# Kernel tuning notes

Measured on AMD Instinct MI355X. Metric: run time of the kernel, lower is better.

The kernel has to match this reference:

```python
import jax, jax.numpy as jnp
import numpy as np

N, T, C, H, W = 4, 8, 512, 14, 14
HEADS = 8
D = C // HEADS            # 64 per-head dim
S = T * H * W             # 1568 sequence length
EPS = 1e-8
NEG = -2.0**32 + 1.0      # padding value used by the original module


def setup_inputs() -> dict:
    key = jax.random.key(0)
    ks = jax.random.split(key, 8)
    shp = (N, T, C, H, W)
    scale = 1.0 / np.sqrt(C)
    return {
        "queries": jax.random.normal(ks[0], shp, jnp.float32),
        "keys": jax.random.normal(ks[1], shp, jnp.float32),
        "values": jax.random.normal(ks[2], shp, jnp.float32),
        "Wq": jax.random.normal(ks[3], (C, C), jnp.float32) * scale,
        "bq": jnp.zeros((C,), jnp.float32),
        "Wk": jax.random.normal(ks[4], (C, C), jnp.float32) * scale,
        "bk": jnp.zeros((C,), jnp.float32),
        "Wv": jax.random.normal(ks[5], (C, C), jnp.float32) * scale,
        "bv": jnp.zeros((C,), jnp.float32),
        "gamma": jnp.ones((C,), jnp.float32),
        "beta": jnp.zeros((C,), jnp.float32),
    }


def _proj(x, Wt, b):
    # 1x1 Conv2d + ReLU over channel dim of (N, T, C, H, W)
    y = jnp.einsum('ntchw,oc->ntohw', x, Wt) + b[None, None, :, None, None]
    return jax.nn.relu(y)


def _flatten(x):
    # (N, T, C, H, W) -> (N, T*H*W, C)
    return x.transpose(0, 1, 3, 4, 2).reshape(N, S, C)


def _split_heads(x):
    # torch.cat(torch.chunk(x, HEADS, dim=2), dim=0): (N, S, C) -> (HEADS*N, S, D)
    return x.reshape(N, S, HEADS, D).transpose(2, 0, 1, 3).reshape(HEADS * N, S, D)


def reference(queries, keys, values, Wq, bq, Wk, bk, Wv, bv, gamma, beta):
    Qf = _flatten(_proj(queries, Wq, bq))
    Kf = _flatten(_proj(keys, Wk, bk))
    Vf = _flatten(_proj(values, Wv, bv))
    q_flat = _flatten(queries)   # residual + query mask source
    k_flat = _flatten(keys)      # key mask source

    Q_ = _split_heads(Qf)
    K_ = _split_heads(Kf)
    V_ = _split_heads(Vf)

    scores = jnp.einsum('bqd,bkd->bqk', Q_, K_) / jnp.sqrt(jnp.float32(D))

    # key padding mask: sign(|sum over C|), tiled over heads -> (HEADS*N, 1, S)
    key_mask = jnp.sign(jnp.abs(k_flat.sum(-1)))          # (N, S)
    km = jnp.tile(key_mask, (HEADS, 1))[:, None, :]
    scores = jnp.where(km == 0.0, NEG, scores)

    attn = jax.nn.softmax(scores, axis=-1)

    # query padding mask (multiplicative) -> (HEADS*N, S, 1)
    query_mask = jnp.sign(jnp.abs(q_flat.sum(-1)))        # (N, S)
    qm = jnp.tile(query_mask, (HEADS, 1))[:, :, None]
    attn = attn * qm

    out = jnp.einsum('bqk,bkd->bqd', attn, V_)
    # merge heads back: inverse of _split_heads
    out = out.reshape(HEADS, N, S, D).transpose(1, 2, 0, 3).reshape(N, S, C)

    out = out + q_flat  # residual

    # custom LayerNorm: torch .std() is unbiased (ddof=1)
    mean = out.mean(-1, keepdims=True)
    std = jnp.sqrt(out.var(-1, ddof=1, keepdims=True))
    out = gamma * (out - mean) / (std + EPS) + beta

    # reshape back to (N, T, C, H, W)
    return out.reshape(N, T, H, W, C).transpose(0, 1, 4, 2, 3)
```

## Files before the change

kernel.cpp:

```cpp
#include <hip/hip_runtime.h>
#include <math.h>

#define N_ 4
#define T_ 8
#define C_ 512
#define H_ 14
#define W_ 14
#define HEADS_ 8
#define D_ 64
#define HW_ 196
#define S_ 1568
#define P_TOT 6272
#define KMP_ 1600
#define NEGL_ (-1.0e38f)
#define EPS_ 1e-8f
#define QSC_ 0.18033688011112042f

typedef __attribute__((ext_vector_type(8))) short short8v;
typedef __attribute__((ext_vector_type(4))) float float4v;
typedef __attribute__((ext_vector_type(4))) unsigned short ushort4v;
typedef unsigned short ushort_t;

__device__ __forceinline__ ushort_t f2bf(float f) {
    union { float f; unsigned u; } a; a.f = f;
    unsigned r = (a.u + 0x7FFFu + ((a.u >> 16) & 1u)) >> 16;
    return (ushort_t)r;
}
__device__ __forceinline__ float bf2f(ushort_t u) {
    union { unsigned u; float f; } t; t.u = ((unsigned)u) << 16; return t.f;
}
__device__ __forceinline__ unsigned cvt_pk_bf16(float lo, float hi) {
    unsigned r;
    asm("v_cvt_pk_bf16_f32 %0, %1, %2" : "=v"(r) : "v"(lo), "v"(hi));
    return r;
}
__device__ __forceinline__ float exp2_fast(float x) {
    float r;
    asm("v_exp_f32 %0, %1" : "=v"(r) : "v"(x));
    return r;
}
__device__ __forceinline__ float max3f(float a, float b, float c) {
    float r;
    asm("v_max3_f32 %0, %1, %2, %3" : "=v"(r) : "v"(a), "v"(b), "v"(c));
    return r;
}
__device__ __forceinline__ float4v mfma16(short8v a, short8v b, float4v c) {
    return __builtin_amdgcn_mfma_f32_16x16x32_bf16(a, b, c, 0, 0, 0);
}
__device__ __forceinline__ void gload_lds16(const void* g, void* l) {
    __builtin_amdgcn_global_load_lds(
        (const __attribute__((address_space(1))) unsigned int*)g,
        (__attribute__((address_space(3))) unsigned int*)l,
        16, 0, 0);
}
__device__ __forceinline__ void gload_lds4(const void* g, void* l) {
    __builtin_amdgcn_global_load_lds(
        (const __attribute__((address_space(1))) unsigned int*)g,
        (__attribute__((address_space(3))) unsigned int*)l,
        4, 0, 0);
}

__global__ __launch_bounds__(256) void transpose_kernel(
    const float* __restrict__ q_in, const float* __restrict__ k_in,
    const float* __restrict__ v_in, ushort_t* __restrict__ qbf,
    ushort_t* __restrict__ kbf, ushort_t* __restrict__ vbf)
{
    __shared__ float Xs[64][197];
    const int z = blockIdx.z;
    const float* src = (z == 0) ? q_in : (z == 1) ? k_in : v_in;
    ushort_t* dst = (z == 0) ? qbf : (z == 1) ? kbf : vbf;

    const int nt = blockIdx.x;
    const int ct = blockIdx.y;
    const int tid = threadIdx.x;

    const long gbase = ((long)nt * C_ + ct * 64) * HW_;
    #pragma unroll
    for (int i = 0; i < 13; ++i) {
        const int idx = i * 256 + tid;
        if (idx < 3136) {
            const int c = idx / 49;
            const int q4 = idx - c * 49;
            const float4 v = *(const float4*)(src + gbase + c * HW_ + q4 * 4);
            Xs[c][q4 * 4 + 0] = v.x;
            Xs[c][q4 * 4 + 1] = v.y;
            Xs[c][q4 * 4 + 2] = v.z;
            Xs[c][q4 * 4 + 3] = v.w;
        }
    }
    __syncthreads();
    const long pbase = (long)nt * HW_;
    const int c0 = (tid & 15) * 4;
    #pragma unroll
    for (int i = 0; i < 13; ++i) {
        const int idx = i * 256 + tid;
        if (idx < 3136) {
            const int hw = idx >> 4;
            ushort4v pk;
            #pragma unroll
            for (int e = 0; e < 4; ++e) pk[e] = f2bf(Xs[c0 + e][hw]);
            *(ushort4v*)(dst + (pbase + hw) * C_ + ct * 64 + c0) = pk;
        }
    }
}

__global__ __launch_bounds__(256) void wconv_kernel(
    const float* __restrict__ Wq, const float* __restrict__ Wk,
    const float* __restrict__ Wv, ushort_t* __restrict__ Wbf)
{
    const int z = blockIdx.y;
    const float* src = (z == 0) ? Wq : (z == 1) ? Wk : Wv;
    const int q = blockIdx.x * 256 + threadIdx.x;
    const float4 v = *(const float4*)(src + q * 4);
    ushort4v pk;
    pk[0] = f2bf(v.x); pk[1] = f2bf(v.y); pk[2] = f2bf(v.z); pk[3] = f2bf(v.w);
    *(ushort4v*)(Wbf + (long)z * 262144 + q * 4) = pk;
}

__global__ __launch_bounds__(256) void mask_kernel(
    const ushort_t* __restrict__ qbf, const ushort_t* __restrict__ kbf,
    float* __restrict__ qm, float* __restrict__ km)
{
    const int tid = threadIdx.x;
    const int w = tid >> 6, lane = tid & 63;
    const int p = blockIdx.x * 4 + w;
    const short8v qv = *(const short8v*)(qbf + (long)p * C_ + lane * 8);
    const short8v kv = *(const short8v*)(kbf + (long)p * C_ + lane * 8);
    float sq = 0.f, sk = 0.f;
    #pragma unroll
    for (int j = 0; j < 8; ++j) {
        sq += bf2f(((const ushort_t*)&qv)[j]);
        sk += bf2f(((const ushort_t*)&kv)[j]);
    }
    #pragma unroll
    for (int off = 32; off > 0; off >>= 1) {
        sq += __shfl_xor(sq, off, 64);
        sk += __shfl_xor(sk, off, 64);
    }
    if (lane == 0) {
        const int n = p / S_, s = p - n * S_;
        qm[p] = (sq != 0.f) ? 1.f : 0.f;
        km[n * KMP_ + s] = (sk != 0.f) ? 0.f : NEGL_;
    }
    if (blockIdx.x == 0 && tid < 128) {
        const int nn = tid >> 5;
        const int ss = S_ + (tid & 31);
        km[nn * KMP_ + ss] = NEGL_;
    }
}

__global__ __launch_bounds__(256) void proj_all(
    const ushort_t* __restrict__ qbf, const ushort_t* __restrict__ kbf,
    const ushort_t* __restrict__ vbf, const ushort_t* __restrict__ Wbf,
    const float* __restrict__ bq, const float* __restrict__ bk,
    const float* __restrict__ bv,
    ushort_t* __restrict__ Qh, ushort_t* __restrict__ Kh,
    ushort_t* __restrict__ Vt)
{
    __shared__ char lds[24576];

    const int fid = blockIdx.x;
    const int xcd = fid & 7;
    const int iin = fid >> 3;
    const int v = xcd * 147 + iin;
    const int z = v / 392;
    const int rem = v - z * 392;
    const int ptile = rem >> 3;
    const int head = rem & 7;

    const ushort_t* Xbf = (z == 0) ? qbf : (z == 1) ? kbf : vbf;
    const ushort_t* Wz = Wbf + (long)z * 262144;
    const float* bias = (z == 0) ? bq : (z == 1) ? bk : bv;
    ushort_t* outp = (z == 0) ? Qh : (z == 1) ? Kh : Vt;
    const bool TR = (z == 2);
    const float osc = (z == 0) ? QSC_ : 1.0f;

    const int tid = threadIdx.x;
    const int w = tid >> 6, lane = tid & 63, lg = lane >> 4, lo = lane & 15;
    const int wr = w >> 1, wc = w & 1;
    const int p0 = ptile * 128;
    const int o0 = head * 64;

    char* Xl = lds;
    char* Wl = lds + 16384;
    const int wbase = (tid & 192) * 16;

    float4v acc[2][4];
    #pragma unroll
    for (int a = 0; a < 2; ++a)
        #pragma unroll
        for (int b = 0; b < 4; ++b) acc[a][b] = (float4v){0.f, 0.f, 0.f, 0.f};

    auto stage = [&](int k0) {
        #pragma unroll
        for (int i = 0; i < 4; ++i) {
            const int sl = tid + i * 256;
            const int row = sl >> 3, sir = sl & 7;
            const int c16 = sir ^ (row & 7);
            gload_lds16(Xbf + (long)(p0 + row) * C_ + k0 + c16 * 8,
                        Xl + i * 4096 + wbase);
        }
        #pragma unroll
        for (int i = 0; i < 2; ++i) {
            const int sl = tid + i * 256;
            const int row = sl >> 3, sir = sl & 7;
            const int c16 = sir ^ (row & 7);
            gload_lds16(Wz + (long)(o0 + row) * C_ + k0 + c16 * 8,
                        Wl + i * 4096 + wbase);
        }
    };

    for (int kstep = 0; kstep < 8; ++kstep) {
        stage(kstep * 64);
        __syncthreads();

        short8v wf[2][2], xf[4][2];
        #pragma unroll
        for (int a = 0; a < 2; ++a) {
            const int row = wc * 32 + a * 16 + lo;
            const int swr = (row & 7) << 4;
            #pragma unroll
            for (int ks = 0; ks < 2; ++ks) {
                const int base = row * 128 + ks * 64 + lg * 8;
                ((uint2*)&wf[a][ks])[0] = *(const uint2*)(Wl + (base ^ swr));
                ((uint2*)&wf[a][ks])[1] = *(const uint2*)(Wl + ((base + 32) ^ swr));
            }
        }
        #pragma unroll
        for (int b = 0; b < 4; ++b) {
            const int row = wr * 64 + b * 16 + lo;
            const int swr = (row & 7) << 4;
            #pragma unroll
            for (int ks = 0; ks < 2; ++ks) {
                const int base = row * 128 + ks * 64 + lg * 8;
                ((uint2*)&xf[b][ks])[0] = *(const uint2*)(Xl + (base ^ swr));
                ((uint2*)&xf[b][ks])[1] = *(const uint2*)(Xl + ((base + 32) ^ swr));
            }
        }
        __builtin_amdgcn_s_setprio(1);
        if (!TR) {
            #pragma unroll
            for (int ks = 0; ks < 2; ++ks)
                #pragma unroll
                for (int a = 0; a < 2; ++a)
                    #pragma unroll
                    for (int b = 0; b < 4; ++b)
                        acc[a][b] = mfma16(wf[a][ks], xf[b][ks], acc[a][b]);
        } else {
            #pragma unroll
            for (int ks = 0; ks < 2; ++ks)
                #pragma unroll
                for (int a = 0; a < 2; ++a)
                    #pragma unroll
                    for (int b = 0; b < 4; ++b)
                        acc[a][b] = mfma16(xf[b][ks], wf[a][ks], acc[a][b]);
        }
        __builtin_amdgcn_s_setprio(0);
        __syncthreads();
    }

    if (!TR) {
        #pragma unroll
        for (int b = 0; b < 4; ++b) {
            const int p = p0 + wr * 64 + b * 16 + lo;
            const int nb = p / S_;
            const int s = p - nb * S_;
            #pragma unroll
            for (int a = 0; a < 2; ++a) {
                const int d0 = wc * 32 + a * 16 + lg * 4;
                const float4v bs = *(const float4v*)(bias + o0 + d0);
                ushort4v pk;
                #pragma unroll
                for (int e = 0; e < 4; ++e) {
                    float vv = acc[a][b][e] + bs[e];
                    vv = vv > 0.f ? vv : 0.f;
                    pk[e] = f2bf(vv * osc);
                }
                *(ushort4v*)(outp + ((long)(head * N_ + nb) * S_ + s) * D_ + d0) = pk;
            }
        }
    } else {
        #pragma unroll
        for (int a = 0; a < 2; ++a) {
            const int d = wc * 32 + a * 16 + lo;
            const float bsc = bias[o0 + d];
            #pragma unroll
            for (int b = 0; b < 4; ++b) {
                const int pb = p0 + wr * 64 + b * 16 + lg * 4;
                const int nb = pb / S_;
                const int s0 = pb - nb * S_;
                ushort4v pk;
                #pragma unroll
                for (int e = 0; e < 4; ++e) {
                    float vv = acc[a][b][e] + bsc;
                    vv = vv > 0.f ? vv : 0.f;
                    pk[e] = f2bf(vv);
                }
                *(ushort4v*)(outp + ((long)(head * N_ + nb) * D_ + d) * S_ + s0) = pk;
            }
        }
    }
}

__global__ __launch_bounds__(256) void attn_kernel(
    const ushort_t* __restrict__ Qh, const ushort_t* __restrict__ Kh,
    const ushort_t* __restrict__ Vt, const float* __restrict__ km,
    ushort_t* __restrict__ Pc, float* __restrict__ Ml)
{
    __shared__ char lds[16384 + 256];

    const int tid = threadIdx.x;
    const int lane = tid & 63;
    const int w = tid >> 6;
    const int lg = lane >> 4;
    const int lo = lane & 15;

    const int split = blockIdx.y;
    const int t1 = 7 + split * 6;
    const int t0 = split ? (1 + split * 6) : 0;

    const int fid = blockIdx.x;
    const int x = fid & 7;
    const int j = fid >> 3;
    const int b = x + 8 * (j / 25);
    const int q0 = (j % 25) * 64;
    const int n = b & (N_ - 1);

    char* Kl = lds;
    char* Vl = lds + 8192;
    const float* kms = (const float*)(lds + 16384);
    const int wbase = (tid & 192) * 16;

    const int qrow = q0 + w * 16 + lo;
    const int qcl = qrow < S_ ? qrow : S_ - 1;
    const ushort_t* qp = Qh + ((long)b * S_ + qcl) * D_ + lg * 4;
    short8v qf[2];
    #pragma unroll
    for (int ks = 0; ks < 2; ++ks) {
        ((uint2*)&qf[ks])[0] = *(const uint2*)(qp + ks * 32);
        ((uint2*)&qf[ks])[1] = *(const uint2*)(qp + ks * 32 + 16);
    }

    float4v acc[4];
    #pragma unroll
    for (int dt = 0; dt < 4; ++dt) acc[dt] = (float4v){0.f, 0.f, 0.f, 0.f};
    float m_run = -INFINITY, l_run = 0.f;

    auto stage = [&](int kb) {
        #pragma unroll
        for (int i = 0; i < 2; ++i) {
            const int s = i * 256 + tid;
            const int row = s >> 3;
            const int c16 = (s & 7) ^ (row & 7);
            int krow = kb + row; if (krow >= S_) krow = S_ - 1;
            gload_lds16(Kh + ((long)b * S_ + krow) * D_ + c16 * 8,
                        Kl + i * 4096 + wbase);
        }
        #pragma unroll
        for (int i = 0; i < 2; ++i) {
            const int s = i * 256 + tid;
            const int row = s >> 3;
            const int c16 = (s & 7) ^ (row & 7);
            int kc = kb + c16 * 8; if (kc > S_ - 8) kc = S_ - 8;
            gload_lds16(Vt + ((long)b * D_ + row) * S_ + kc,
                        Vl + i * 4096 + wbase);
        }
        if (w == 0)
            gload_lds4(km + (long)n * KMP_ + kb + lane, (void*)kms);
    };

    for (int t = t0; t < t1; ++t) {
        stage(t * 64);
        __syncthreads();

        float4v s[4];
        __builtin_amdgcn_s_setprio(1);
        #pragma unroll
        for (int kt = 0; kt < 4; ++kt) {
            s[kt] = (float4v){0.f, 0.f, 0.f, 0.f};
            #pragma unroll
            for (int ks = 0; ks < 2; ++ks) {
                const int row = kt * 16 + lo;
                const int base = row * 128 + ks * 64 + lg * 8;
                const int swr = (row & 7) << 4;
                short8v kf;
                ((uint2*)&kf)[0] = *(const uint2*)(Kl + (base ^ swr));
                ((uint2*)&kf)[1] = *(const uint2*)(Kl + ((base + 32) ^ swr));
                s[kt] = mfma16(kf, qf[ks], s[kt]);
            }
        }
        __builtin_amdgcn_s_setprio(0);

        float p[4][4];
        #pragma unroll
        for (int kt = 0; kt < 4; ++kt) {
            const float4v bv4 = *(const float4v*)&kms[kt * 16 + lg * 4];
            #pragma unroll
            for (int r = 0; r < 4; ++r) p[kt][r] = s[kt][r] + bv4[r];
        }
        const float m1 = max3f(p[0][0], p[0][1], p[0][2]);
        const float m2 = max3f(p[0][3], p[1][0], p[1][1]);
        const float m3 = max3f(p[1][2], p[1][3], p[2][0]);
        const float m4 = max3f(p[2][1], p[2][2], p[2][3]);
        const float m5 = max3f(p[3][0], p[3][1], p[3][2]);
        float mx = max3f(max3f(m1, m2, m3), m4, fmaxf(m5, p[3][3]));
        mx = fmaxf(mx, __shfl_xor(mx, 16, 64));
        mx = fmaxf(mx, __shfl_xor(mx, 32, 64));
        float mn;
        if (__all(mx <= m_run + 8.f)) {
            mn = m_run;
        } else {
            mn = fmaxf(m_run, mx);
            const float alpha = exp2_fast(m_run - mn);
            m_run = mn;
            l_run *= alpha;
            #pragma unroll
            for (int dt = 0; dt < 4; ++dt)
                #pragma unroll
                for (int r = 0; r < 4; ++r) acc[dt][r] *= alpha;
        }
        float rs4[4];
        #pragma unroll
        for (int kt = 0; kt < 4; ++kt) {
            #pragma unroll
            for (int r = 0; r < 4; ++r) p[kt][r] = exp2_fast(p[kt][r] - mn);
            rs4[kt] = (p[kt][0] + p[kt][1]) + (p[kt][2] + p[kt][3]);
        }
        l_run += (rs4[0] + rs4[1]) + (rs4[2] + rs4[3]);

        short8v pf[2];
        #pragma unroll
        for (int kt = 0; kt < 4; ++kt) {
            const unsigned w0 = cvt_pk_bf16(p[kt][0], p[kt][1]);
            const unsigned w1 = cvt_pk_bf16(p[kt][2], p[kt][3]);
            ((unsigned*)&pf[kt >> 1])[(kt & 1) * 2] = w0;
            ((unsigned*)&pf[kt >> 1])[(kt & 1) * 2 + 1] = w1;
        }

        __builtin_amdgcn_s_setprio(1);
        #pragma unroll
        for (int dt = 0; dt < 4; ++dt) {
            #pragma unroll
            for (int ks = 0; ks < 2; ++ks) {
                const int row = dt * 16 + lo;
                const int base = row * 128 + ks * 64 + lg * 8;
                const int swr = (row & 7) << 4;
                short8v vf;
                ((uint2*)&vf)[0] = *(const uint2*)(Vl + (base ^ swr));
                ((uint2*)&vf)[1] = *(const uint2*)(Vl + ((base + 32) ^ swr));
                acc[dt] = mfma16(vf, pf[ks], acc[dt]);
            }
        }
        __builtin_amdgcn_s_setprio(0);
        __syncthreads();
    }

    l_run += __shfl_xor(l_run, 16, 64);
    l_run += __shfl_xor(l_run, 32, 64);

    if (qrow < S_) {
        const long rbase = ((long)split * 32 + b) * S_ + qrow;
        if (lg == 0) {
            Ml[rbase * 2] = m_run;
            Ml[rbase * 2 + 1] = l_run;
        }
        ushort_t* P = Pc + rbase * 64;
        #pragma unroll
        for (int dt = 0; dt < 4; ++dt) {
            uint2 uu;
            uu.x = cvt_pk_bf16(acc[dt][0], acc[dt][1]);
            uu.y = cvt_pk_bf16(acc[dt][2], acc[dt][3]);
            *(uint2*)(P + dt * 16 + lg * 4) = uu;
        }
    }
}

__global__ __launch_bounds__(256) void combine_stats_kernel(
    const ushort_t* __restrict__ Pc, const float* __restrict__ Ml,
    const float* __restrict__ qm, const ushort_t* __restrict__ qbf,
    ushort_t* __restrict__ Om, float* __restrict__ stats)
{
    const int tid = threadIdx.x;
    const int wv = tid >> 6, lane = tid & 63;
    const long pos = (long)blockIdx.x * 4 + wv;
    const int n = (int)(pos / S_);
    const int q = (int)(pos - (long)n * S_);
    const int head = lane >> 3;
    const int d0 = (lane & 7) * 8;

    long rb[4];
    float mv[4], lv[4];
    float M = -INFINITY;
    #pragma unroll
    for (int s = 0; s < 4; ++s) {
        rb[s] = ((long)(s * 32 + head * 4 + n) * S_ + q);
        const float2 ml = *(const float2*)(Ml + rb[s] * 2);
        mv[s] = ml.x; lv[s] = ml.y;
        M = fmaxf(M, ml.x);
    }
    float L = 0.f;
    float o[8] = {0.f, 0.f, 0.f, 0.f, 0.f, 0.f, 0.f, 0.f};
    #pragma unroll
    for (int s = 0; s < 4; ++s) {
        const float wgt = exp2_fast(mv[s] - M);
        L = fmaf(lv[s], wgt, L);
        const ushort4v a0 = *(const ushort4v*)(Pc + rb[s] * 64 + d0);
        const ushort4v a1 = *(const ushort4v*)(Pc + rb[s] * 64 + d0 + 4);
        #pragma unroll
        for (int e = 0; e < 4; ++e) {
            o[e] = fmaf(bf2f(a0[e]), wgt, o[e]);
            o[4 + e] = fmaf(bf2f(a1[e]), wgt, o[4 + e]);
        }
    }
    L = fmaxf(L, 1e-20f);
    const float scale = qm[pos] / L;
    const short8v qv = *(const short8v*)(qbf + pos * C_ + lane * 8);
    ushort4v ov0, ov1;
    float sum = 0.f, ssq = 0.f;
    #pragma unroll
    for (int e = 0; e < 8; ++e) {
        const ushort_t ob = f2bf(o[e] * scale);
        if (e < 4) ov0[e] = ob; else ov1[e - 4] = ob;
        const float v = bf2f(ob) + bf2f(((const ushort_t*)&qv)[e]);
        sum += v; ssq += v * v;
    }
    #pragma unroll
    for (int off = 32; off > 0; off >>= 1) {
        sum += __shfl_xor(sum, off, 64);
        ssq += __shfl_xor(ssq, off, 64);
    }
    *(ushort4v*)(Om + pos * C_ + lane * 8) = ov0;
    *(ushort4v*)(Om + pos * C_ + lane * 8 + 4) = ov1;
    if (lane == 0) {
        const float mean = sum * (1.f / 512.f);
        float var = (ssq - sum * mean) * (1.f / 511.f);
        var = var > 0.f ? var : 0.f;
        stats[pos * 2] = mean;
        stats[pos * 2 + 1] = 1.f / (sqrtf(var) + EPS_);
    }
}

__global__ __launch_bounds__(256) void ln_write_kernel(
    const ushort_t* __restrict__ Om, const ushort_t* __restrict__ qbf,
    const float* __restrict__ stats, const float* __restrict__ gamma,
    const float* __restrict__ beta, float* __restrict__ out)
{
    __shared__ float Tl[64][197];
    const int nt = blockIdx.x;
    const int ct = blockIdx.y;
    const int tid = threadIdx.x;

    const int c0 = (tid & 15) * 4;
    float g[4], bb[4];
    #pragma unroll
    for (int e = 0; e < 4; ++e) {
        g[e] = gamma[ct * 64 + c0 + e];
        bb[e] = beta[ct * 64 + c0 + e];
    }

    #pragma unroll
    for (int i = 0; i < 13; ++i) {
        const int idx = i * 256 + tid;
        if (idx < 3136) {
            const int hw = idx >> 4;
            const long p = (long)nt * HW_ + hw;
            const float mean = stats[p * 2];
            const float inv = stats[p * 2 + 1];
            const ushort4v ov = *(const ushort4v*)(Om + p * C_ + ct * 64 + c0);
            const ushort4v qv = *(const ushort4v*)(qbf + p * C_ + ct * 64 + c0);
            #pragma unroll
            for (int e = 0; e < 4; ++e) {
                const float xv = bf2f(ov[e]) + bf2f(qv[e]);
                Tl[c0 + e][hw] = g[e] * (xv - mean) * inv + bb[e];
            }
        }
    }
    __syncthreads();
    const long obase = ((long)nt * C_ + ct * 64) * HW_;
    #pragma unroll
    for (int i = 0; i < 13; ++i) {
        const int idx = i * 256 + tid;
        if (idx < 3136) {
            const int c = idx / 49;
            const int q4 = idx - c * 49;
            float4 v;
            v.x = Tl[c][q4 * 4 + 0];
            v.y = Tl[c][q4 * 4 + 1];
            v.z = Tl[c][q4 * 4 + 2];
            v.w = Tl[c][q4 * 4 + 3];
            *(float4*)(out + obase + c * HW_ + q4 * 4) = v;
        }
    }
}

extern "C" void kernel_launch(void* const* d_in, const int* in_sizes, int n_in,
                              void* d_out, int out_size, void* d_ws, size_t ws_size,
                              hipStream_t stream) {
    const float* q_in  = (const float*)d_in[0];
    const float* k_in  = (const float*)d_in[1];
    const float* v_in  = (const float*)d_in[2];
    const float* Wq    = (const float*)d_in[3];
    const float* bq    = (const float*)d_in[4];
    const float* Wk    = (const float*)d_in[5];
    const float* bk    = (const float*)d_in[6];
    const float* Wv    = (const float*)d_in[7];
    const float* bv    = (const float*)d_in[8];
    const float* gamma = (const float*)d_in[9];
    const float* beta  = (const float*)d_in[10];
    float* out = (float*)d_out;

    const size_t PC = (size_t)P_TOT * C_;
    ushort_t* qbf = (ushort_t*)d_ws;
    ushort_t* kbf = qbf + PC;
    ushort_t* vbf = kbf + PC;
    ushort_t* Wbf = vbf + PC;
    ushort_t* Qh  = Wbf + 3 * (size_t)C_ * C_;
    ushort_t* Kh  = Qh + PC;
    ushort_t* Vt  = Kh + PC;
    ushort_t* Om  = Vt + PC;
    ushort_t* Pc  = Om + PC;
    float* Ml    = (float*)(Pc + 4L * 32 * S_ * 64);
    float* stats = Ml + 4L * 32 * S_ * 2;
    float* qm    = stats + 2 * P_TOT;
    float* km    = qm + P_TOT;

    transpose_kernel<<<dim3(32, 8, 3), 256, 0, stream>>>(q_in, k_in, v_in, qbf, kbf, vbf);
    wconv_kernel<<<dim3(256, 3), 256, 0, stream>>>(Wq, Wk, Wv, Wbf);
    mask_kernel<<<P_TOT / 4, 256, 0, stream>>>(qbf, kbf, qm, km);
    proj_all<<<1176, 256, 0, stream>>>(qbf, kbf, vbf, Wbf, bq, bk, bv, Qh, Kh, Vt);
    attn_kernel<<<dim3(800, 4), 256, 0, stream>>>(Qh, Kh, Vt, km, Pc, Ml);
    combine_stats_kernel<<<P_TOT / 4, 256, 0, stream>>>(Pc, Ml, qm, qbf, Om, stats);
    ln_write_kernel<<<dim3(32, 8), 256, 0, stream>>>(Om, qbf, stats, gamma, beta, out);
}
```

Before: 103.7 us.

## Double-buffer K/V tiles in attention kernel and preload key mask once

Attention kernel now uses two LDS buffers for K and V, issuing the async global-to-LDS load for the next key tile before computing on the current one, with one barrier per tile. The key-mask bias for the block's whole key range is loaded into LDS once at kernel start rather than per tile. Swizzled LDS fragment offsets are precomputed once. The goal is to hide global load latency behind MFMA work; the cost is doubled LDS use, which may reduce occupancy.

```diff
diff --git a/kernel.cpp b/kernel.cpp
--- a/kernel.cpp
+++ b/kernel.cpp
@@ -53,12 +53,6 @@
         (__attribute__((address_space(3))) unsigned int*)l,
         16, 0, 0);
 }
-__device__ __forceinline__ void gload_lds4(const void* g, void* l) {
-    __builtin_amdgcn_global_load_lds(
-        (const __attribute__((address_space(1))) unsigned int*)g,
-        (__attribute__((address_space(3))) unsigned int*)l,
-        4, 0, 0);
-}
 
 __global__ __launch_bounds__(256) void transpose_kernel(
     const float* __restrict__ q_in, const float* __restrict__ k_in,
@@ -307,7 +301,7 @@
     const ushort_t* __restrict__ Vt, const float* __restrict__ km,
     ushort_t* __restrict__ Pc, float* __restrict__ Ml)
 {
-    __shared__ char lds[16384 + 256];
+    __shared__ char lds[2 * 16384 + 1792];
 
     const int tid = threadIdx.x;
     const int lane = tid & 63;
@@ -326,10 +320,17 @@
     const int q0 = (j % 25) * 64;
     const int n = b & (N_ - 1);
 
-    char* Kl = lds;
-    char* Vl = lds + 8192;
-    const float* kms = (const float*)(lds + 16384);
     const int wbase = (tid & 192) * 16;
+    float* kml = (float*)(lds + 32768);
+
+    {
+        const int nt = (t1 - t0) * 64;
+        #pragma unroll
+        for (int i = 0; i < 2; ++i) {
+            const int idx = i * 256 + tid;
+            if (idx < nt) kml[idx] = km[(long)n * KMP_ + t0 * 64 + idx];
+        }
+    }
 
     const int qrow = q0 + w * 16 + lo;
     const int qcl = qrow < S_ ? qrow : S_ - 1;
@@ -346,7 +347,12 @@
     for (int dt = 0; dt < 4; ++dt) acc[dt] = (float4v){0.f, 0.f, 0.f, 0.f};
     float m_run = -INFINITY, l_run = 0.f;
 
-    auto stage = [&](int kb) {
+    const int swr = (lo & 7) << 4;
+    const int fo[2][2] = {
+        { ((lg * 8) ^ swr) + lo * 128,      ((lg * 8 + 32) ^ swr) + lo * 128 },
+        { ((64 + lg * 8) ^ swr) + lo * 128, ((64 + lg * 8 + 32) ^ swr) + lo * 128 } };
+
+    auto stage = [&](char* Kb, char* Vb, int kb) {
         #pragma unroll
         for (int i = 0; i < 2; ++i) {
             const int s = i * 256 + tid;
@@ -354,7 +360,7 @@
             const int c16 = (s & 7) ^ (row & 7);
             int krow = kb + row; if (krow >= S_) krow = S_ - 1;
             gload_lds16(Kh + ((long)b * S_ + krow) * D_ + c16 * 8,
-                        Kl + i * 4096 + wbase);
+                        Kb + i * 4096 + wbase);
         }
         #pragma unroll
         for (int i = 0; i < 2; ++i) {
@@ -363,15 +369,15 @@
             const int c16 = (s & 7) ^ (row & 7);
             int kc = kb + c16 * 8; if (kc > S_ - 8) kc = S_ - 8;
             gload_lds16(Vt + ((long)b * D_ + row) * S_ + kc,
-                        Vl + i * 4096 + wbase);
-        }
-        if (w == 0)
-            gload_lds4(km + (long)n * KMP_ + kb + lane, (void*)kms);
+                        Vb + i * 4096 + wbase);
+        }
     };
 
-    for (int t = t0; t < t1; ++t) {
-        stage(t * 64);
-        __syncthreads();
+    char* K0 = lds;             char* V0 = lds + 8192;
+    char* K1 = lds + 16384;     char* V1 = lds + 24576;
+
+    auto compute = [&](const char* Kl, const char* Vl, int t) {
+        const float* kms = kml + (t - t0) * 64;
 
         float4v s[4];
         __builtin_amdgcn_s_setprio(1);
@@ -380,12 +386,9 @@
             s[kt] = (float4v){0.f, 0.f, 0.f, 0.f};
             #pragma unroll
             for (int ks = 0; ks < 2; ++ks) {
-                const int row = kt * 16 + lo;
-                const int base = row * 128 + ks * 64 + lg * 8;
-                const int swr = (row & 7) << 4;
                 short8v kf;
-                ((uint2*)&kf)[0] = *(const uint2*)(Kl + (base ^ swr));
-                ((uint2*)&kf)[1] = *(const uint2*)(Kl + ((base + 32) ^ swr));
+                ((uint2*)&kf)[0] = *(const uint2*)(Kl + kt * 2048 + fo[ks][0]);
+                ((uint2*)&kf)[1] = *(const uint2*)(Kl + kt * 2048 + fo[ks][1]);
                 s[kt] = mfma16(kf, qf[ks], s[kt]);
             }
         }
@@ -442,17 +445,24 @@
         for (int dt = 0; dt < 4; ++dt) {
             #pragma unroll
             for (int ks = 0; ks < 2; ++ks) {
-                const int row = dt * 16 + lo;
-                const int base = row * 128 + ks * 64 + lg * 8;
-                const int swr = (row & 7) << 4;
                 short8v vf;
-                ((uint2*)&vf)[0] = *(const uint2*)(Vl + (base ^ swr));
-                ((uint2*)&vf)[1] = *(const uint2*)(Vl + ((base + 32) ^ swr));
+                ((uint2*)&vf)[0] = *(const uint2*)(Vl + dt * 2048 + fo[ks][0]);
+                ((uint2*)&vf)[1] = *(const uint2*)(Vl + dt * 2048 + fo[ks][1]);
                 acc[dt] = mfma16(vf, pf[ks], acc[dt]);
             }
         }
         __builtin_amdgcn_s_setprio(0);
+    };
+
+    stage(K0, V0, t0 * 64);
+    for (int t = t0; t < t1; t += 2) {
         __syncthreads();
+        if (t + 1 < t1) stage(K1, V1, (t + 1) * 64);
+        compute(K0, V0, t);
+        if (t + 1 >= t1) break;
+        __syncthreads();
+        if (t + 2 < t1) stage(K0, V0, (t + 2) * 64);
+        compute(K1, V1, t + 1);
     }
 
     l_run += __shfl_xor(l_run, 16, 64);
```

Result: slower. 114.5 us (+10.5%).

## Double-buffer projection GEMM LDS staging and fold weight conversion into transpose

Applied to the files above, without the earlier changes.

The projection GEMM now uses two LDS buffers, issuing the global-to-LDS load for the next k-step before computing on the current one. This removes one barrier per iteration and overlaps load latency with MFMA work. Separately, the weight fp32->bf16 conversion is merged into the transpose kernel as an extra z-slice, which saves one kernel launch. LDS use per block doubles to 48KB, which may lower occupancy.

```diff
diff --git a/kernel.cpp b/kernel.cpp
--- a/kernel.cpp
+++ b/kernel.cpp
@@ -63,16 +63,35 @@
 __global__ __launch_bounds__(256) void transpose_kernel(
     const float* __restrict__ q_in, const float* __restrict__ k_in,
     const float* __restrict__ v_in, ushort_t* __restrict__ qbf,
-    ushort_t* __restrict__ kbf, ushort_t* __restrict__ vbf)
+    ushort_t* __restrict__ kbf, ushort_t* __restrict__ vbf,
+    const float* __restrict__ Wq, const float* __restrict__ Wk,
+    const float* __restrict__ Wv, ushort_t* __restrict__ Wbf)
 {
     __shared__ float Xs[64][197];
     const int z = blockIdx.z;
-    const float* src = (z == 0) ? q_in : (z == 1) ? k_in : v_in;
-    ushort_t* dst = (z == 0) ? qbf : (z == 1) ? kbf : vbf;
-
     const int nt = blockIdx.x;
     const int ct = blockIdx.y;
     const int tid = threadIdx.x;
+
+    if (z == 3) {
+        const int blk = nt * 8 + ct;
+        #pragma unroll
+        for (int i = 0; i < 3; ++i) {
+            const int q = (blk * 3 + i) * 256 + tid;
+            const int zi = q >> 16;
+            const int qi = q & 65535;
+            const float* src = (zi == 0) ? Wq : (zi == 1) ? Wk : Wv;
+            const float4 v = *(const float4*)(src + qi * 4);
+            ushort4v pk;
+            pk[0] = f2bf(v.x); pk[1] = f2bf(v.y);
+            pk[2] = f2bf(v.z); pk[3] = f2bf(v.w);
+            *(ushort4v*)(Wbf + (long)zi * 262144 + qi * 4) = pk;
+        }
+        return;
+    }
+
+    const float* src = (z == 0) ? q_in : (z == 1) ? k_in : v_in;
+    ushort_t* dst = (z == 0) ? qbf : (z == 1) ? kbf : vbf;
 
     const long gbase = ((long)nt * C_ + ct * 64) * HW_;
     #pragma unroll
@@ -104,19 +123,6 @@
     }
 }
 
-__global__ __launch_bounds__(256) void wconv_kernel(
-    const float* __restrict__ Wq, const float* __restrict__ Wk,
-    const float* __restrict__ Wv, ushort_t* __restrict__ Wbf)
-{
-    const int z = blockIdx.y;
-    const float* src = (z == 0) ? Wq : (z == 1) ? Wk : Wv;
-    const int q = blockIdx.x * 256 + threadIdx.x;
-    const float4 v = *(const float4*)(src + q * 4);
-    ushort4v pk;
-    pk[0] = f2bf(v.x); pk[1] = f2bf(v.y); pk[2] = f2bf(v.z); pk[3] = f2bf(v.w);
-    *(ushort4v*)(Wbf + (long)z * 262144 + q * 4) = pk;
-}
-
 __global__ __launch_bounds__(256) void mask_kernel(
     const ushort_t* __restrict__ qbf, const ushort_t* __restrict__ kbf,
     float* __restrict__ qm, float* __restrict__ km)
@@ -157,7 +163,7 @@
     ushort_t* __restrict__ Qh, ushort_t* __restrict__ Kh,
     ushort_t* __restrict__ Vt)
 {
-    __shared__ char lds[24576];
+    __shared__ char lds[49152];
 
     const int fid = blockIdx.x;
     const int xcd = fid & 7;
@@ -181,8 +187,6 @@
     const int p0 = ptile * 128;
     const int o0 = head * 64;
 
-    char* Xl = lds;
-    char* Wl = lds + 16384;
     const int wbase = (tid & 192) * 16;
 
     float4v acc[2][4];
@@ -191,7 +195,9 @@
         #pragma unroll
         for (int b = 0; b < 4; ++b) acc[a][b] = (float4v){0.f, 0.f, 0.f, 0.f};
 
-    auto stage = [&](int k0) {
+    auto stage = [&](int buf, int k0) {
+        char* Xl = lds + buf * 24576;
+        char* Wl = Xl + 16384;
         #pragma unroll
         for (int i = 0; i < 4; ++i) {
             const int sl = tid + i * 256;
@@ -210,10 +216,14 @@
         }
     };
 
+    stage(0, 0);
+    #pragma unroll
     for (int kstep = 0; kstep < 8; ++kstep) {
-        stage(kstep * 64);
         __syncthreads();
-
+        if (kstep < 7) stage((kstep + 1) & 1, (kstep + 1) * 64);
+
+        const char* Xl = lds + (kstep & 1) * 24576;
+        const char* Wl = Xl + 16384;
         short8v wf[2][2], xf[4][2];
         #pragma unroll
         for (int a = 0; a < 2; ++a) {
@@ -256,7 +266,6 @@
                         acc[a][b] = mfma16(xf[b][ks], wf[a][ks], acc[a][b]);
         }
         __builtin_amdgcn_s_setprio(0);
-        __syncthreads();
     }
 
     if (!TR) {
@@ -624,8 +633,8 @@
     float* qm    = stats + 2 * P_TOT;
     float* km    = qm + P_TOT;
 
-    transpose_kernel<<<dim3(32, 8, 3), 256, 0, stream>>>(q_in, k_in, v_in, qbf, kbf, vbf);
-    wconv_kernel<<<dim3(256, 3), 256, 0, stream>>>(Wq, Wk, Wv, Wbf);
+    transpose_kernel<<<dim3(32, 8, 4), 256, 0, stream>>>(
+        q_in, k_in, v_in, qbf, kbf, vbf, Wq, Wk, Wv, Wbf);
     mask_kernel<<<P_TOT / 4, 256, 0, stream>>>(qbf, kbf, qm, km);
     proj_all<<<1176, 256, 0, stream>>>(qbf, kbf, vbf, Wbf, bq, bk, bv, Qh, Kh, Vt);
     attn_kernel<<<dim3(800, 4), 256, 0, stream>>>(Qh, Kh, Vt, km, Pc, Ml);
```

Result: faster. 101.5 us (-2.1%).
